# Kernel tuning notes

Hardware: AMD Instinct MI355X
Metric: run time of the kernel (lower is better)

Reference implementation:

```python
import jax, jax.numpy as jnp
import numpy as np

D_MODEL = 1024
N_HEADS = 16
D_HIDDEN = 4096
EPS = 1e-6
MASK_VAL = 1e10


def layernorm(x, gamma, beta):
    # Matches torch module: unbiased std (N-1), divide by (std + eps)
    mean = jnp.mean(x, axis=-1, keepdims=True)
    d = x.shape[-1]
    std = jnp.sqrt(jnp.sum((x - mean) ** 2, axis=-1, keepdims=True) / (d - 1))
    return gamma * (x - mean) / (std + EPS) + beta


def multihead(q_in, k_in, v_in, wq, wk, wv, wo, causal):
    # nn.Linear(bias=False): y = x @ W.T
    q = q_in @ wq.T
    k = k_in @ wk.T
    v = v_in @ wv.T
    B, Sq, D = q.shape
    Sk = k.shape[1]
    H, dh = N_HEADS, D // N_HEADS
    q = q.reshape(B, Sq, H, dh)
    k = k.reshape(B, Sk, H, dh)
    v = v.reshape(B, Sk, H, dh)
    scores = jnp.einsum('bqhd,bkhd->bhqk', q, k)  # [B,H,Sq,Sk]
    if causal:
        tri = jnp.triu(jnp.full((Sk, Sk), MASK_VAL, dtype=scores.dtype), k=1)
        scores = scores - tri  # mask applied BEFORE scaling, as in source
    scale = jnp.sqrt(jnp.asarray(D_MODEL, dtype=scores.dtype))  # d_key = d_model
    att = jax.nn.softmax(scores / scale, axis=-1)
    out = jnp.einsum('bhqk,bkhd->bqhd', att, v).reshape(B, Sq, D)
    return out @ wo.T


def setup_inputs() -> dict:
    key = jax.random.key(0)
    ks = jax.random.split(key, 24)
    B, S, D, DH = 2, 2048, D_MODEL, D_HIDDEN
    w = lambda k, shp: (jax.random.normal(k, shp, dtype=jnp.float32) * 0.02)
    inp = {
        'x': jax.random.normal(ks[0], (B, S, D), dtype=jnp.float32),
        'encoding': jax.random.normal(ks[1], (B, S, D), dtype=jnp.float32),
        'sa_wq': w(ks[2], (D, D)), 'sa_wk': w(ks[3], (D, D)),
        'sa_wv': w(ks[4], (D, D)), 'sa_wo': w(ks[5], (D, D)),
        'ca_wq': w(ks[6], (D, D)), 'ca_wk': w(ks[7], (D, D)),
        'ca_wv': w(ks[8], (D, D)), 'ca_wo': w(ks[9], (D, D)),
        'ff_w1': w(ks[10], (DH, D)), 'ff_b1': jnp.zeros((DH,), jnp.float32),
        'ff_w2': w(ks[11], (D, DH)), 'ff_b2': jnp.zeros((D,), jnp.float32),
        'ln1_g': jnp.ones((D,), jnp.float32), 'ln1_b': jnp.zeros((D,), jnp.float32),
        'ln2_g': jnp.ones((D,), jnp.float32), 'ln2_b': jnp.zeros((D,), jnp.float32),
        'ln3_g': jnp.ones((D,), jnp.float32), 'ln3_b': jnp.zeros((D,), jnp.float32),
    }
    return inp


def reference(x, encoding, sa_wq, sa_wk, sa_wv, sa_wo, ca_wq, ca_wk, ca_wv, ca_wo,
              ff_w1, ff_b1, ff_w2, ff_b2, ln1_g, ln1_b, ln2_g, ln2_b, ln3_g, ln3_b):
    # self-attention (causal) + post-norm residual
    h = layernorm(x + multihead(x, x, x, sa_wq, sa_wk, sa_wv, sa_wo, causal=True), ln1_g, ln1_b)
    # cross-attention + post-norm residual
    h = layernorm(h + multihead(h, encoding, encoding, ca_wq, ca_wk, ca_wv, ca_wo, causal=False), ln2_g, ln2_b)
    # feed-forward + post-norm residual
    ff = jax.nn.relu(h @ ff_w1.T + ff_b1) @ ff_w2.T + ff_b2
    return layernorm(h + ff, ln3_g, ln3_b)
```

## Files before the change

kernel.cpp:

```cpp
#include <hip/hip_runtime.h>
#include <hip/hip_bf16.h>
#include <math.h>

#define D_MODEL 1024
#define NHEADS  16
#define DHEAD   64
#define D_HID   4096

typedef __attribute__((ext_vector_type(8))) short short8;
typedef __attribute__((ext_vector_type(4))) short short4v;
typedef __attribute__((ext_vector_type(4))) float f32x4;
typedef __attribute__((ext_vector_type(16))) float f32x16;

#define QSCALE_F 0.04508422002778011f
#define MASK_T   4.5084220e8f

__device__ inline short f2bs(float x) {
    union { __hip_bfloat16 b; short s; } u;
    u.b = __float2bfloat16(x);
    return u.s;
}
__device__ inline float bs2f(ushort s) {
    union { unsigned u; float f; } v; v.u = ((unsigned)s) << 16; return v.f;
}
__device__ inline unsigned cvtpk(float lo, float hi) {
    unsigned r;
    asm("v_cvt_pk_bf16_f32 %0, %1, %2" : "=v"(r) : "v"(lo), "v"(hi));
    return r;
}
__device__ inline short8 pack8(float4 x, float4 y) {
    short8 v;
    v[0] = f2bs(x.x); v[1] = f2bs(x.y); v[2] = f2bs(x.z); v[3] = f2bs(x.w);
    v[4] = f2bs(y.x); v[5] = f2bs(y.y); v[6] = f2bs(y.z); v[7] = f2bs(y.w);
    return v;
}
typedef const unsigned __attribute__((address_space(1))) gu32;
typedef unsigned __attribute__((address_space(3))) lu32;
__device__ inline void gload16(const void* g, void* l) {
    __builtin_amdgcn_global_load_lds((gu32*)g, (lu32*)l, 16, 0, 0);
}
__device__ inline int swz(int r, int byteInRow) {
    return (r * 128 + byteInRow) ^ ((r & 7) << 4);
}

struct WP { const float* p[10]; };
__global__ __launch_bounds__(256) void cast_weights(WP wp, short* __restrict__ dst) {
    const int n8 = (16 << 20) / 8;
    for (int i = blockIdx.x * 256 + threadIdx.x; i < n8; i += gridDim.x * 256) {
        size_t e = (size_t)i * 8;
        int seg = (int)(e >> 20);
        const float* src;
        if (seg < 8)       src = wp.p[seg] + (e & ((1u << 20) - 1));
        else if (seg < 12) src = wp.p[8] + (e - ((size_t)8 << 20));
        else               src = wp.p[9] + (e - ((size_t)12 << 20));
        float4 a = *(const float4*)src;
        float4 b = *(const float4*)(src + 4);
        *(short8*)(dst + e) = pack8(a, b);
    }
}

__global__ __launch_bounds__(256) void cast_f2b(const float* __restrict__ in,
                                                short* __restrict__ out, int n8) {
    for (int i = blockIdx.x * 256 + threadIdx.x; i < n8; i += gridDim.x * 256) {
        float4 a = *(const float4*)(in + (size_t)i * 8);
        float4 b = *(const float4*)(in + (size_t)i * 8 + 4);
        *(short8*)(out + (size_t)i * 8) = pack8(a, b);
    }
}

template<int OM, bool BIAS, bool RELU, bool ACCUM>
__global__ __launch_bounds__(512) void gemm_mfma(
    const short* __restrict__ A, int lda,
    const short* __restrict__ Bm, int ldb,
    const float* __restrict__ bias,
    float* __restrict__ Cf, short* __restrict__ Cb, int ldc,
    int M, int N, int K, size_t routeElems, float qscale)
{
    __shared__ short Als[2][128 * 64];
    __shared__ short Bls[2][128 * 64];

    const int tid = threadIdx.x, w = tid >> 6, l = tid & 63;
    const int l15 = l & 15, lhi = l >> 4;
    const int wr = w >> 2, wc = w & 3;

    const int kh = (OM == 3) ? blockIdx.z : 0;
    if (OM == 3) {
        A  += (size_t)kh * K;
        Bm += (size_t)kh * K;
    }

    const unsigned nwg  = gridDim.x * gridDim.y;
    const unsigned wgid = blockIdx.y * gridDim.x + blockIdx.x;
    const unsigned cpx  = nwg >> 3;
    const unsigned sid  = (wgid & 7) * cpx + (wgid >> 3);
    const int bm = (int)(sid / gridDim.x) * 128;
    const int bn = (int)(sid % gridDim.x) * 128;

    const int srow = w * 8 + (l >> 3);
    const int schk = ((l & 7) ^ (l >> 3)) * 8;

    f32x4 acc[4][2] = {};

    #pragma unroll
    for (int i = 0; i < 2; ++i) {
        const short* ga = A  + (size_t)(bm + i * 64 + srow) * lda + schk;
        const short* gb = Bm + (size_t)(bn + i * 64 + srow) * ldb + schk;
        gload16(ga, &Als[0][i * 4096 + w * 512 + l * 8]);
        gload16(gb, &Bls[0][i * 4096 + w * 512 + l * 8]);
    }
    __syncthreads();

    const int nIter = K >> 6;
    int cur = 0;
    for (int it = 0; it < nIter; ++it) {
        if (it + 1 < nIter) {
            const int k1 = (it + 1) << 6;
            #pragma unroll
            for (int i = 0; i < 2; ++i) {
                const short* ga = A  + (size_t)(bm + i * 64 + srow) * lda + k1 + schk;
                const short* gb = Bm + (size_t)(bn + i * 64 + srow) * ldb + k1 + schk;
                gload16(ga, &Als[cur ^ 1][i * 4096 + w * 512 + l * 8]);
                gload16(gb, &Bls[cur ^ 1][i * 4096 + w * 512 + l * 8]);
            }
        }

        short8 af[4][2], bf[2][2];
        #pragma unroll
        for (int m = 0; m < 4; ++m) {
            const int row = wr * 64 + m * 16 + l15;
            #pragma unroll
            for (int kk = 0; kk < 2; ++kk)
                af[m][kk] = *(const short8*)&Als[cur][row * 64 + (((kk * 4 + lhi) ^ (l15 & 7)) * 8)];
        }
        #pragma unroll
        for (int n = 0; n < 2; ++n) {
            const int row = wc * 32 + n * 16 + l15;
            #pragma unroll
            for (int kk = 0; kk < 2; ++kk)
                bf[n][kk] = *(const short8*)&Bls[cur][row * 64 + (((kk * 4 + lhi) ^ (l15 & 7)) * 8)];
        }
        __builtin_amdgcn_s_setprio(1);
        #pragma unroll
        for (int kk = 0; kk < 2; ++kk)
            #pragma unroll
            for (int m = 0; m < 4; ++m)
                #pragma unroll
                for (int n = 0; n < 2; ++n)
                    acc[m][n] = __builtin_amdgcn_mfma_f32_16x16x32_bf16(af[m][kk], bf[n][kk], acc[m][n], 0, 0, 0);
        __builtin_amdgcn_s_setprio(0);

        __syncthreads();
        cur ^= 1;
    }

    #pragma unroll
    for (int n = 0; n < 2; ++n) {
        const int col = bn + wc * 32 + n * 16 + l15;
        float bv = 0.f;
        if (BIAS && (OM != 3 || kh == 0)) bv = bias[col];
        const float sc = (OM == 2) ? (col < 1024 ? qscale : 1.f) : qscale;
        #pragma unroll
        for (int m = 0; m < 4; ++m) {
            const int row0 = bm + wr * 64 + m * 16 + lhi * 4;
            #pragma unroll
            for (int i = 0; i < 4; ++i) {
                float v = acc[m][n][i] + bv;
                if (ACCUM) v += Cf[(size_t)(row0 + i) * ldc + col];
                if (RELU)  v = fmaxf(v, 0.f);
                v *= sc;
                if (OM == 0) {
                    Cf[(size_t)(row0 + i) * ldc + col] = v;
                } else if (OM == 1) {
                    Cb[(size_t)(row0 + i) * ldc + col] = f2bs(v);
                } else if (OM == 2) {
                    Cb[(size_t)(col >> 10) * routeElems +
                       (size_t)(row0 + i) * 1024 + (col & 1023)] = f2bs(v);
                } else {
                    if (kh == 0) Cf[(size_t)(row0 + i) * ldc + col] = v;
                    else         Cb[(size_t)(row0 + i) * ldc + col] = f2bs(v);
                }
            }
        }
    }
}

__global__ __launch_bounds__(256) void v_prep(
    const short* __restrict__ Vb_, short* __restrict__ Vt, int S)
{
    const int t = blockIdx.x, bh = blockIdx.y;
    const int b = bh >> 4, h = bh & 15;
    const int tid = threadIdx.x;
    const int r = tid >> 2, g = tid & 3;
    __shared__ ushort vs[64][65];

    const size_t inrow = ((size_t)b * S + t * 64 + r) * D_MODEL + h * DHEAD;
    const size_t tbase = ((size_t)bh * (S / 64) + t) * 4096;

    short8 v0 = *(const short8*)(Vb_ + inrow + g * 16);
    short8 v1 = *(const short8*)(Vb_ + inrow + g * 16 + 8);
    #pragma unroll
    for (int j = 0; j < 8; ++j) { vs[r][g * 16 + j] = (ushort)v0[j]; vs[r][g * 16 + 8 + j] = (ushort)v1[j]; }
    __syncthreads();
    short8 q0, q1;
    #pragma unroll
    for (int j = 0; j < 8; ++j) {
        q0[j] = (short)vs[g * 16 + j][r];
        q1[j] = (short)vs[g * 16 + 8 + j][r];
    }
    *(short8*)(Vt + tbase + r * 64 + g * 16)     = q0;
    *(short8*)(Vt + tbase + r * 64 + g * 16 + 8) = q1;
}

template<bool CAUSAL>
__global__ __launch_bounds__(512) void attn_v13(
    const short* __restrict__ Qb, const short* __restrict__ Kr,
    const short* __restrict__ Vt, short* __restrict__ Out, int S)
{
    __shared__ __align__(16) char smem[2 * 16384];

    const int tid = threadIdx.x, w = tid >> 6, l = tid & 63;
    const int l31 = l & 31, hi = l >> 5;

    const unsigned wgid = blockIdx.y * gridDim.x + blockIdx.x;
    const unsigned sid  = (wgid & 7) * 32 + (wgid >> 3);
    const int bnd = (int)(sid & 7);
    const int bh  = (int)(sid >> 3);
    const int b = bh >> 4, h = bh & 15;
    const int qw = bnd * 256 + w * 32;
    const int q  = qw + l31;

    const short* qp = Qb + ((size_t)(b * S + q)) * 1024 + h * 64 + hi * 8;
    short8 bq[4];
    #pragma unroll
    for (int dc = 0; dc < 4; ++dc) bq[dc] = *(const short8*)(qp + dc * 16);

    const short* kbase = Kr + ((size_t)b * S) * 1024 + h * 64;
    const short* vbase = Vt + (size_t)bh * ((S / 64) * 4096);

    f32x16 ot0 = {}, ot1 = {};
    float l_lane = 0.f;

    const int tMax = CAUSAL ? (4 * bnd + 3) : (S / 64 - 1);

    const int sro  = w * 8 + (l >> 3);
    const int schk = ((l & 7) ^ (l >> 3)) * 8;

    {
        char* Kls = smem;  char* Vls = smem + 8192;
        gload16(kbase + (size_t)sro * 1024 + schk, Kls + (size_t)w * 1024);
        gload16(vbase + (size_t)sro * 64   + schk, Vls + (size_t)w * 1024);
    }
    __syncthreads();

    int cur = 0;
    for (int t = 0; t <= tMax; ++t) {
        if (t + 1 <= tMax) {
            char* Kn = smem + (cur ^ 1) * 16384;
            char* Vn = Kn + 8192;
            gload16(kbase + (size_t)((t + 1) * 64 + sro) * 1024 + schk, Kn + (size_t)w * 1024);
            gload16(vbase + (size_t)(t + 1) * 4096 + (size_t)sro * 64 + schk, Vn + (size_t)w * 1024);
        }

        const char* Kls = smem + cur * 16384;
        const char* Vls = Kls + 8192;
        const int kv0 = t * 64;

        if (!(CAUSAL && kv0 > qw + 31)) {
            f32x16 st0 = {}, st1 = {};
            __builtin_amdgcn_s_setprio(1);
            #pragma unroll
            for (int dc = 0; dc < 4; ++dc) {
                short8 a0 = *(const short8*)(Kls + swz(l31,      dc * 32 + hi * 16));
                short8 a1 = *(const short8*)(Kls + swz(32 + l31, dc * 32 + hi * 16));
                st0 = __builtin_amdgcn_mfma_f32_32x32x16_bf16(a0, bq[dc], st0, 0, 0, 0);
                st1 = __builtin_amdgcn_mfma_f32_32x32x16_bf16(a1, bq[dc], st1, 0, 0, 0);
            }
            __builtin_amdgcn_s_setprio(0);

            if (CAUSAL && kv0 + 31 > qw) {
                #pragma unroll
                for (int r = 0; r < 16; ++r) {
                    int kv = kv0 + (r & 3) + 8 * (r >> 2) + 4 * hi;
                    if (kv > q) st0[r] -= MASK_T;
                }
            }
            if (CAUSAL && kv0 + 63 > qw) {
                #pragma unroll
                for (int r = 0; r < 16; ++r) {
                    int kv = kv0 + 32 + (r & 3) + 8 * (r >> 2) + 4 * hi;
                    if (kv > q) st1[r] -= MASK_T;
                }
            }

            union U { unsigned u[4]; short8 s; };
            U c00, c01, c10, c11;
            {
                float p[16];
                #pragma unroll
                for (int r = 0; r < 16; ++r) { p[r] = __builtin_amdgcn_exp2f(st0[r]); l_lane += p[r]; }
                unsigned wd[8], sx[8];
                #pragma unroll
                for (int i = 0; i < 8; ++i) wd[i] = cvtpk(p[2 * i], p[2 * i + 1]);
                #pragma unroll
                for (int i = 0; i < 8; ++i) sx[i] = __shfl_xor(wd[i], 32, 64);
                if (hi == 0) {
                    c00.u[0] = wd[0]; c00.u[1] = wd[1]; c00.u[2] = sx[0]; c00.u[3] = sx[1];
                    c01.u[0] = wd[4]; c01.u[1] = wd[5]; c01.u[2] = sx[4]; c01.u[3] = sx[5];
                } else {
                    c00.u[0] = sx[2]; c00.u[1] = sx[3]; c00.u[2] = wd[2]; c00.u[3] = wd[3];
                    c01.u[0] = sx[6]; c01.u[1] = sx[7]; c01.u[2] = wd[6]; c01.u[3] = wd[7];
                }
            }
            {
                float p[16];
                #pragma unroll
                for (int r = 0; r < 16; ++r) { p[r] = __builtin_amdgcn_exp2f(st1[r]); l_lane += p[r]; }
                unsigned wd[8], sx[8];
                #pragma unroll
                for (int i = 0; i < 8; ++i) wd[i] = cvtpk(p[2 * i], p[2 * i + 1]);
                #pragma unroll
                for (int i = 0; i < 8; ++i) sx[i] = __shfl_xor(wd[i], 32, 64);
                if (hi == 0) {
                    c10.u[0] = wd[0]; c10.u[1] = wd[1]; c10.u[2] = sx[0]; c10.u[3] = sx[1];
                    c11.u[0] = wd[4]; c11.u[1] = wd[5]; c11.u[2] = sx[4]; c11.u[3] = sx[5];
                } else {
                    c10.u[0] = sx[2]; c10.u[1] = sx[3]; c10.u[2] = wd[2]; c10.u[3] = wd[3];
                    c11.u[0] = sx[6]; c11.u[1] = sx[7]; c11.u[2] = wd[6]; c11.u[3] = wd[7];
                }
            }

            __builtin_amdgcn_s_setprio(1);
            short8 av;
            av  = *(const short8*)(Vls + swz(l31,      hi * 16));
            ot0 = __builtin_amdgcn_mfma_f32_32x32x16_bf16(av, c00.s, ot0, 0, 0, 0);
            av  = *(const short8*)(Vls + swz(32 + l31, hi * 16));
            ot1 = __builtin_amdgcn_mfma_f32_32x32x16_bf16(av, c00.s, ot1, 0, 0, 0);
            av  = *(const short8*)(Vls + swz(l31,      32 + hi * 16));
            ot0 = __builtin_amdgcn_mfma_f32_32x32x16_bf16(av, c01.s, ot0, 0, 0, 0);
            av  = *(const short8*)(Vls + swz(32 + l31, 32 + hi * 16));
            ot1 = __builtin_amdgcn_mfma_f32_32x32x16_bf16(av, c01.s, ot1, 0, 0, 0);
            av  = *(const short8*)(Vls + swz(l31,      64 + hi * 16));
            ot0 = __builtin_amdgcn_mfma_f32_32x32x16_bf16(av, c10.s, ot0, 0, 0, 0);
            av  = *(const short8*)(Vls + swz(32 + l31, 64 + hi * 16));
            ot1 = __builtin_amdgcn_mfma_f32_32x32x16_bf16(av, c10.s, ot1, 0, 0, 0);
            av  = *(const short8*)(Vls + swz(l31,      96 + hi * 16));
            ot0 = __builtin_amdgcn_mfma_f32_32x32x16_bf16(av, c11.s, ot0, 0, 0, 0);
            av  = *(const short8*)(Vls + swz(32 + l31, 96 + hi * 16));
            ot1 = __builtin_amdgcn_mfma_f32_32x32x16_bf16(av, c11.s, ot1, 0, 0, 0);
            __builtin_amdgcn_s_setprio(0);
        }

        __syncthreads();
        cur ^= 1;
    }

    const float l_tot = l_lane + __shfl_xor(l_lane, 32, 64);
    const float inv = 1.f / l_tot;
    short* orow = Out + ((size_t)(b * S + q)) * 1024 + h * 64;
    #pragma unroll
    for (int i = 0; i < 8; ++i) {
        int dbase = ((2 * i) & 3) + 8 * (i >> 1) + 4 * hi;
        *(unsigned*)(orow + dbase)      = cvtpk(ot0[2 * i] * inv, ot0[2 * i + 1] * inv);
        *(unsigned*)(orow + 32 + dbase) = cvtpk(ot1[2 * i] * inv, ot1[2 * i + 1] * inv);
    }
}

template<bool IN1BF, bool OUTBF, bool P3>
__global__ __launch_bounds__(256) void add_ln(
    const void* __restrict__ in1, const float* __restrict__ in2,
    const short* __restrict__ in3,
    const float* __restrict__ gam, const float* __restrict__ bet,
    void* __restrict__ y)
{
    const int row = blockIdx.x;
    const int tid = threadIdx.x;
    const size_t off = (size_t)row * D_MODEL;

    float a0, a1, a2, a3;
    if (IN1BF) {
        short4v xs = ((const short4v*)((const short*)in1 + off))[tid];
        a0 = bs2f((ushort)xs[0]); a1 = bs2f((ushort)xs[1]);
        a2 = bs2f((ushort)xs[2]); a3 = bs2f((ushort)xs[3]);
    } else {
        float4 xv = ((const float4*)((const float*)in1 + off))[tid];
        a0 = xv.x; a1 = xv.y; a2 = xv.z; a3 = xv.w;
    }
    float4 rv = ((const float4*)(in2 + off))[tid];
    float v0 = a0 + rv.x, v1 = a1 + rv.y, v2 = a2 + rv.z, v3 = a3 + rv.w;
    if (P3) {
        short4v ps = ((const short4v*)(in3 + off))[tid];
        v0 += bs2f((ushort)ps[0]); v1 += bs2f((ushort)ps[1]);
        v2 += bs2f((ushort)ps[2]); v3 += bs2f((ushort)ps[3]);
    }

    float s  = v0 + v1 + v2 + v3;
    float ss = v0 * v0 + v1 * v1 + v2 * v2 + v3 * v3;

    __shared__ float sb[8];
    #pragma unroll
    for (int o = 32; o > 0; o >>= 1) {
        s  += __shfl_down(s, o, 64);
        ss += __shfl_down(ss, o, 64);
    }
    const int lane = tid & 63, w = tid >> 6;
    if (lane == 0) { sb[w] = s; sb[4 + w] = ss; }
    __syncthreads();
    float S  = sb[0] + sb[1] + sb[2] + sb[3];
    float SS = sb[4] + sb[5] + sb[6] + sb[7];

    float mean = S * (1.f / D_MODEL);
    float var_sum = SS - S * mean;
    float stdv = sqrtf(var_sum * (1.f / (D_MODEL - 1)));
    float inv = 1.f / (stdv + 1e-6f);

    float4 gv = ((const float4*)gam)[tid];
    float4 bv = ((const float4*)bet)[tid];
    float o0 = gv.x * (v0 - mean) * inv + bv.x;
    float o1 = gv.y * (v1 - mean) * inv + bv.y;
    float o2 = gv.z * (v2 - mean) * inv + bv.z;
    float o3 = gv.w * (v3 - mean) * inv + bv.w;
    if (OUTBF) {
        short4v ov; ov[0] = f2bs(o0); ov[1] = f2bs(o1); ov[2] = f2bs(o2); ov[3] = f2bs(o3);
        ((short4v*)((short*)y + off))[tid] = ov;
    } else {
        ((float4*)((float*)y + off))[tid] = make_float4(o0, o1, o2, o3);
    }
}

extern "C" void kernel_launch(void* const* d_in, const int* in_sizes, int n_in,
                              void* d_out, int out_size, void* d_ws, size_t ws_size,
                              hipStream_t stream)
{
    const float* x     = (const float*)d_in[0];
    const float* enc   = (const float*)d_in[1];
    WP wp;
    for (int i = 0; i < 8; ++i) wp.p[i] = (const float*)d_in[2 + i];
    wp.p[8] = (const float*)d_in[10];
    wp.p[9] = (const float*)d_in[12];
    const float* ff_b1 = (const float*)d_in[11];
    const float* ff_b2 = (const float*)d_in[13];
    const float* ln1_g = (const float*)d_in[14];
    const float* ln1_b = (const float*)d_in[15];
    const float* ln2_g = (const float*)d_in[16];
    const float* ln2_b = (const float*)d_in[17];
    const float* ln3_g = (const float*)d_in[18];
    const float* ln3_b = (const float*)d_in[19];
    float* out = (float*)d_out;

    const int Bn = 2, S = 2048, M = Bn * S;
    const size_t MB = 1u << 20;
    char* ws = (char*)d_ws;
    short* Wb   = (short*)(ws);
    short* p32  = (short*)(ws + 32 * MB);
    short* p40  = (short*)(ws + 40 * MB);
    short* p48  = (short*)(ws + 48 * MB);
    short* p56  = (short*)(ws + 56 * MB);
    short* p64  = (short*)(ws + 64 * MB);
    short* p72  = (short*)(ws + 72 * MB);
    float* f0   = (float*)(ws + 80 * MB);

    short* tbuf = p48;

    const size_t RT = 4 * MB;
    const short* W_saqkv = Wb;
    const short* W_sawo  = Wb + 3 * MB;
    const short* W_caq   = Wb + 4 * MB;
    const short* W_cakv  = Wb + 5 * MB;
    const short* W_cawo  = Wb + 7 * MB;
    const short* W_ff1   = Wb + 8 * MB;
    const short* W_ff2   = Wb + 12 * MB;

    dim3 blk(256);
    dim3 blk512(512);
    dim3 g_qkv(3072 / 128, M / 128);
    dim3 g_kv(2048 / 128, M / 128);
    dim3 g_n1k(1024 / 128, M / 128);
    dim3 g_spl(1024 / 128, M / 128, 2);
    dim3 g_ff1(4096 / 128, M / 128);
    dim3 g_attn(S / 256, Bn * NHEADS);
    dim3 g_vp(S / 64, Bn * NHEADS);
    dim3 g_ln(M);

    cast_weights<<<2048, blk, 0, stream>>>(wp, Wb);
    cast_f2b<<<2048, blk, 0, stream>>>(x, p32, (M * D_MODEL) / 8);

    gemm_mfma<2,false,false,false><<<g_qkv, blk512, 0, stream>>>(p32, 1024, W_saqkv, 1024, nullptr, nullptr, p40, 1024, M, 3072, 1024, RT, QSCALE_F);
    v_prep<<<g_vp, blk, 0, stream>>>(p56, p72, S);
    attn_v13<true><<<g_attn, blk512, 0, stream>>>(p40, p48, p72, p32, S);
    gemm_mfma<3,false,false,false><<<g_spl, blk512, 0, stream>>>(p32, 1024, W_sawo, 1024, nullptr, f0, p48, 1024, M, 1024, 512, 0, 1.f);
    add_ln<false,true,true><<<g_ln, blk, 0, stream>>>(x, f0, p48, ln1_g, ln1_b, p32);

    cast_f2b<<<2048, blk, 0, stream>>>(enc, p64, (M * D_MODEL) / 8);
    gemm_mfma<2,false,false,false><<<g_kv, blk512, 0, stream>>>(p64, 1024, W_cakv, 1024, nullptr, nullptr, p48, 1024, M, 2048, 1024, RT, 1.f);
    gemm_mfma<1,false,false,false><<<g_n1k, blk512, 0, stream>>>(p32, 1024, W_caq, 1024, nullptr, nullptr, p40, 1024, M, 1024, 1024, 0, QSCALE_F);
    v_prep<<<g_vp, blk, 0, stream>>>(p56, p72, S);
    attn_v13<false><<<g_attn, blk512, 0, stream>>>(p40, p48, p72, p56, S);
    gemm_mfma<3,false,false,false><<<g_spl, blk512, 0, stream>>>(p56, 1024, W_cawo, 1024, nullptr, f0, p48, 1024, M, 1024, 512, 0, 1.f);
    add_ln<true,true,true><<<g_ln, blk, 0, stream>>>(p32, f0, p48, ln2_g, ln2_b, p40);

    gemm_mfma<1,true,true,false><<<g_ff1, blk512, 0, stream>>>(p40, 1024, W_ff1, 1024, ff_b1, nullptr, tbuf, 4096, M, 4096, 1024, 0, 1.f);
    gemm_mfma<3,true,false,false><<<g_spl, blk512, 0, stream>>>(tbuf, 4096, W_ff2, 4096, ff_b2, f0, p32, 1024, M, 1024, 2048, 0, 1.f);
    add_ln<true,false,true><<<g_ln, blk, 0, stream>>>(p40, f0, p32, ln3_g, ln3_b, out);
}
```

Before: 345.5 us.

## Triple-buffer GEMM LDS tiles with two-deep prefetch and vmcnt waits

Grows the MFMA GEMM's shared-memory staging from double to triple buffering, issuing global-to-LDS loads two K-iterations ahead. Each iteration waits with a partial s_waitcnt vmcnt(4) plus a raw barrier instead of a full __syncthreads, so one prefetch stays in flight during compute. The goal is to hide global load latency better. The cost is 96KB of LDS per block, which may lower occupancy, and correctness now depends on the vmcnt count matching the number of loads each thread issues.

```diff
diff --git a/kernel.cpp b/kernel.cpp
--- a/kernel.cpp
+++ b/kernel.cpp
@@ -76,8 +76,8 @@
     float* __restrict__ Cf, short* __restrict__ Cb, int ldc,
     int M, int N, int K, size_t routeElems, float qscale)
 {
-    __shared__ short Als[2][128 * 64];
-    __shared__ short Bls[2][128 * 64];
+    __shared__ short Als[3][128 * 64];
+    __shared__ short Bls[3][128 * 64];
 
     const int tid = threadIdx.x, w = tid >> 6, l = tid & 63;
     const int l15 = l & 15, lhi = l >> 4;
@@ -100,27 +100,33 @@
     const int schk = ((l & 7) ^ (l >> 3)) * 8;
 
     f32x4 acc[4][2] = {};
+    const int nIter = K >> 6;
 
     #pragma unroll
     for (int i = 0; i < 2; ++i) {
-        const short* ga = A  + (size_t)(bm + i * 64 + srow) * lda + schk;
-        const short* gb = Bm + (size_t)(bn + i * 64 + srow) * ldb + schk;
-        gload16(ga, &Als[0][i * 4096 + w * 512 + l * 8]);
-        gload16(gb, &Bls[0][i * 4096 + w * 512 + l * 8]);
-    }
-    __syncthreads();
-
-    const int nIter = K >> 6;
-    int cur = 0;
+        gload16(A  + (size_t)(bm + i * 64 + srow) * lda + schk, &Als[0][i * 4096 + w * 512 + l * 8]);
+        gload16(Bm + (size_t)(bn + i * 64 + srow) * ldb + schk, &Bls[0][i * 4096 + w * 512 + l * 8]);
+    }
+    if (1 < nIter) {
+        #pragma unroll
+        for (int i = 0; i < 2; ++i) {
+            gload16(A  + (size_t)(bm + i * 64 + srow) * lda + 64 + schk, &Als[1][i * 4096 + w * 512 + l * 8]);
+            gload16(Bm + (size_t)(bn + i * 64 + srow) * ldb + 64 + schk, &Bls[1][i * 4096 + w * 512 + l * 8]);
+        }
+        asm volatile("s_waitcnt vmcnt(4)" ::: "memory");
+    } else {
+        asm volatile("s_waitcnt vmcnt(0)" ::: "memory");
+    }
+    __builtin_amdgcn_s_barrier();
+
+    int cur = 0, nxt2 = 2;
     for (int it = 0; it < nIter; ++it) {
-        if (it + 1 < nIter) {
-            const int k1 = (it + 1) << 6;
+        if (it + 2 < nIter) {
+            const int k2 = (it + 2) << 6;
             #pragma unroll
             for (int i = 0; i < 2; ++i) {
-                const short* ga = A  + (size_t)(bm + i * 64 + srow) * lda + k1 + schk;
-                const short* gb = Bm + (size_t)(bn + i * 64 + srow) * ldb + k1 + schk;
-                gload16(ga, &Als[cur ^ 1][i * 4096 + w * 512 + l * 8]);
-                gload16(gb, &Bls[cur ^ 1][i * 4096 + w * 512 + l * 8]);
+                gload16(A  + (size_t)(bm + i * 64 + srow) * lda + k2 + schk, &Als[nxt2][i * 4096 + w * 512 + l * 8]);
+                gload16(Bm + (size_t)(bn + i * 64 + srow) * ldb + k2 + schk, &Bls[nxt2][i * 4096 + w * 512 + l * 8]);
             }
         }
 
@@ -149,8 +155,15 @@
                     acc[m][n] = __builtin_amdgcn_mfma_f32_16x16x32_bf16(af[m][kk], bf[n][kk], acc[m][n], 0, 0, 0);
         __builtin_amdgcn_s_setprio(0);
 
-        __syncthreads();
-        cur ^= 1;
+        if (it + 2 < nIter) {
+            asm volatile("s_waitcnt vmcnt(4)" ::: "memory");
+            __builtin_amdgcn_s_barrier();
+        } else if (it + 1 < nIter) {
+            asm volatile("s_waitcnt vmcnt(0)" ::: "memory");
+            __builtin_amdgcn_s_barrier();
+        }
+        cur  = (cur  == 2) ? 0 : cur  + 1;
+        nxt2 = (nxt2 == 2) ? 0 : nxt2 + 1;
     }
 
     #pragma unroll
```

New measurement: 444.5 us. +28.6%, slower.
